# Kernel tuning notes

Measured on AMD Instinct MI355X. Metric: run time of the kernel, lower is better.

## Reference

```python
import jax, jax.numpy as jnp
import numpy as np

B, IMG, PATCH = 32, 128, 8
D, H, L, MLP, NC = 512, 8, 8, 2048, 3
P = (IMG // PATCH) ** 2  # 256 patches
N = P + 1                # +cls token
HD = D // H


def layer_norm(x, g, b, eps=1e-5):
    mu = jnp.mean(x, -1, keepdims=True)
    var = jnp.mean((x - mu) ** 2, -1, keepdims=True)
    return (x - mu) * jax.lax.rsqrt(var + eps) * g + b


def spt(x, w, b, g, beta):
    s = 1
    shifts = [x,
              jnp.roll(x, (s, s), (2, 3)),
              jnp.roll(x, (-s, s), (2, 3)),
              jnp.roll(x, (s, -s), (2, 3)),
              jnp.roll(x, (-s, -s), (2, 3))]
    xs = jnp.concatenate(shifts, axis=1)  # (B,5,H,W)
    y = jax.lax.conv_general_dilated(
        xs, w, (PATCH, PATCH), 'VALID',
        dimension_numbers=('NCHW', 'OIHW', 'NCHW')) + b[None, :, None, None]
    tok = y.reshape(y.shape[0], D, -1).transpose(0, 2, 1)  # (B,P,D)
    return layer_norm(tok, g, beta)


def block(tok, p):
    ln1g, ln1b, qkvw, qkvb, projw, projb, temp, ln2g, ln2b, w1, b1, w2, b2 = p
    x = layer_norm(tok, ln1g, ln1b)
    qkv = (x @ qkvw + qkvb).reshape(x.shape[0], N, 3, H, HD)
    q = jnp.transpose(qkv[:, :, 0], (0, 2, 1, 3))  # (B,H,N,HD)
    k = jnp.transpose(qkv[:, :, 1], (0, 2, 1, 3))
    v = jnp.transpose(qkv[:, :, 2], (0, 2, 1, 3))
    attn = jnp.einsum('bhnd,bhmd->bhnm', q, k) * temp[None, :, None, None]
    attn = jnp.where(jnp.eye(N, dtype=bool)[None, None], -jnp.inf, attn)
    attn = jax.nn.softmax(attn, -1)
    o = jnp.einsum('bhnm,bhmd->bhnd', attn, v)
    o = jnp.transpose(o, (0, 2, 1, 3)).reshape(x.shape[0], N, D)
    tok = tok + o @ projw + projb
    y = layer_norm(tok, ln2g, ln2b)
    y = jax.nn.gelu(y @ w1 + b1, approximate=False) @ w2 + b2
    return tok + y


def setup_inputs() -> dict:
    key = jax.random.key(0)
    ks = jax.random.split(key, 16)
    sc = 0.02
    inp = dict(
        image=jax.random.uniform(ks[0], (B, 1, IMG, IMG), jnp.float32),
        ssw=jax.random.normal(ks[1], (D, 5, PATCH, PATCH), jnp.float32) * sc,
        ssb=jnp.zeros((D,), jnp.float32),
        ssg=jnp.ones((D,), jnp.float32),
        ssbeta=jnp.zeros((D,), jnp.float32),
        sow=jax.random.normal(ks[2], (D, 5, PATCH, PATCH), jnp.float32) * sc,
        sob=jnp.zeros((D,), jnp.float32),
        sog=jnp.ones((D,), jnp.float32),
        sobeta=jnp.zeros((D,), jnp.float32),
        fw=jax.random.normal(ks[3], (2 * D, D), jnp.float32) * sc,
        fb=jnp.zeros((D,), jnp.float32),
        cls_token=jax.random.normal(ks[4], (1, 1, D), jnp.float32) * sc,
        pos_embed=jax.random.normal(ks[5], (1, N, D), jnp.float32) * sc,
        ln1g=jnp.ones((L, D), jnp.float32),
        ln1b=jnp.zeros((L, D), jnp.float32),
        qkvw=jax.random.normal(ks[6], (L, D, 3 * D), jnp.float32) * sc,
        qkvb=jnp.zeros((L, 3 * D), jnp.float32),
        projw=jax.random.normal(ks[7], (L, D, D), jnp.float32) * sc,
        projb=jnp.zeros((L, D), jnp.float32),
        temp=jnp.ones((L, H), jnp.float32) / np.sqrt(HD),
        ln2g=jnp.ones((L, D), jnp.float32),
        ln2b=jnp.zeros((L, D), jnp.float32),
        w1=jax.random.normal(ks[8], (L, D, MLP), jnp.float32) * sc,
        b1=jnp.zeros((L, MLP), jnp.float32),
        w2=jax.random.normal(ks[9], (L, MLP, D), jnp.float32) * sc,
        b2=jnp.zeros((L, D), jnp.float32),
        ng=jnp.ones((D,), jnp.float32),
        nb=jnp.zeros((D,), jnp.float32),
        hw=jax.random.normal(ks[10], (D, NC), jnp.float32) * sc,
        hb=jnp.zeros((NC,), jnp.float32),
    )
    return inp


def reference(image, ssw, ssb, ssg, ssbeta, sow, sob, sog, sobeta, fw, fb,
              cls_token, pos_embed, ln1g, ln1b, qkvw, qkvb, projw, projb,
              temp, ln2g, ln2b, w1, b1, w2, b2, ng, nb, hw, hb):
    # InverseLensLayer is undefined in the source repo snippet: identity
    source = image
    src_tok = spt(source, ssw, ssb, ssg, ssbeta)   # (B,P,D)
    orig_tok = spt(image, sow, sob, sog, sobeta)   # (B,P,D)
    comb = jnp.concatenate([src_tok, orig_tok], -1)
    gate = jax.nn.sigmoid(comb @ fw + fb)
    fused = gate * src_tok + (1.0 - gate) * orig_tok
    cls = jnp.broadcast_to(cls_token, (image.shape[0], 1, D))
    tokens = jnp.concatenate([cls, fused], axis=1) + pos_embed  # (B,N,D)

    def body(tok, p):
        return block(tok, p), None

    params = (ln1g, ln1b, qkvw, qkvb, projw, projb, temp,
              ln2g, ln2b, w1, b1, w2, b2)
    tokens, _ = jax.lax.scan(body, tokens, params)
    cls_out = layer_norm(tokens[:, 0], ng, nb)
    logits = cls_out @ hw + hb
    return logits
```

## Files before the change

### kernel.cpp

```cpp
#include <hip/hip_runtime.h>
#include <math.h>

constexpr int B_ = 32, D_ = 512, H_ = 8, L_ = 8, MLP_ = 2048, NC_ = 3;
constexpr int P_ = 256;
constexpr int N_ = 257;
constexpr int HD_ = 64;
constexpr int BP_ = B_ * P_;
constexpr int BN_ = B_ * N_;
constexpr int MP_ = 8320;
constexpr int KP_ = 320;
constexpr int NV_ = 288;

enum { EPI_BIAS = 0, EPI_RES = 1, EPI_GELU = 2 };

using bf16x8 = __attribute__((ext_vector_type(8))) short;
using f32x4  = __attribute__((ext_vector_type(4))) float;

__device__ __forceinline__ float b2f(unsigned short u) {
    return __uint_as_float(((unsigned)u) << 16);
}
__device__ __forceinline__ unsigned short f2b(float f) {
    unsigned u = __float_as_uint(f);
    unsigned r = (u + 0x7FFFu + ((u >> 16) & 1u)) >> 16;
    return (unsigned short)r;
}

__device__ __forceinline__ void gld_lds16(const void* g, void* l) {
    __builtin_amdgcn_global_load_lds(
        (const __attribute__((address_space(1))) void*)g,
        (__attribute__((address_space(3))) void*)l, 16, 0, 0);
}

__global__ void im2col_k(const float* __restrict__ img,
                         unsigned short* __restrict__ X) {
    int idx = blockIdx.x * 256 + threadIdx.x;
    if (idx >= BP_ * KP_) return;
    int r = idx / KP_, j = idx % KP_;
    int b = r >> 8, p = r & 255;
    int py = p >> 4, px = p & 15;
    int c = j >> 6, kk = j & 63;
    int ky = kk >> 3, kx = kk & 7;
    const int dy[5] = {0, 1, -1, 1, -1};
    const int dx[5] = {0, 1, 1, -1, -1};
    int yy = (py * 8 + ky - dy[c] + 128) & 127;
    int xx = (px * 8 + kx - dx[c] + 128) & 127;
    X[idx] = f2b(img[b * 16384 + yy * 128 + xx]);
}

__global__ __launch_bounds__(256) void castT_k(const float* __restrict__ in,
                                               unsigned short* __restrict__ out,
                                               int K, int N) {
    __shared__ float t[32][33];
    size_t loff = (size_t)blockIdx.z * K * N;
    int k0 = blockIdx.x * 32, n0 = blockIdx.y * 32;
    int tx = threadIdx.x & 31, ty = threadIdx.x >> 5;
    for (int i = ty; i < 32; i += 8)
        t[i][tx] = in[loff + (size_t)(k0 + i) * N + n0 + tx];
    __syncthreads();
    for (int i = ty; i < 32; i += 8)
        out[loff + (size_t)(n0 + i) * K + k0 + tx] = f2b(t[tx][i]);
}

__global__ void cast_k(const float* __restrict__ in,
                       unsigned short* __restrict__ out, int n) {
    int idx = blockIdx.x * 256 + threadIdx.x;
    if (idx < n) out[idx] = f2b(in[idx]);
}

__global__ __launch_bounds__(256) void gemm_bf16_k(
    const unsigned short* __restrict__ A, const unsigned short* __restrict__ Bt,
    const float* __restrict__ bias, const float* __restrict__ res,
    float* __restrict__ outF, unsigned short* __restrict__ outB,
    int Nn, int K, int epi) {
    constexpr int BK = 32;
    __shared__ unsigned short As[128 * BK];
    __shared__ unsigned short Bs[128 * BK];
    int tid = threadIdx.x, lane = tid & 63;
    int wave = tid >> 6;
    int wrow = (wave >> 1) * 64, wcol = (wave & 1) * 64;
    size_t bm = (size_t)blockIdx.y * 128, bn = (size_t)blockIdx.x * 128;
    const unsigned short* Ab = A + bm * K;
    const unsigned short* Bb = Bt + bn * K;

    f32x4 acc[4][4] = {};
    int quad = lane >> 4, col = lane & 15;
    int q8 = quad * 8;

    for (int k0 = 0; k0 < K; k0 += BK) {
#pragma unroll
        for (int it = 0; it < 2; ++it) {
            int c = it * 256 + tid;
            int row = c >> 2, cb = (c & 3) * 8;
            gld_lds16(Ab + (size_t)row * K + k0 + cb, (char*)As + c * 16);
            gld_lds16(Bb + (size_t)row * K + k0 + cb, (char*)Bs + c * 16);
        }
        __syncthreads();
        bf16x8 af[4], bfr[4];
#pragma unroll
        for (int i = 0; i < 4; ++i) {
            af[i]  = *(const bf16x8*)&As[(wrow + i * 16 + col) * BK + q8];
            bfr[i] = *(const bf16x8*)&Bs[(wcol + i * 16 + col) * BK + q8];
        }
#pragma unroll
        for (int mi = 0; mi < 4; ++mi)
#pragma unroll
            for (int ni = 0; ni < 4; ++ni)
                acc[mi][ni] = __builtin_amdgcn_mfma_f32_16x16x32_bf16(
                    af[mi], bfr[ni], acc[mi][ni], 0, 0, 0);
        __syncthreads();
    }

#pragma unroll
    for (int mi = 0; mi < 4; ++mi) {
#pragma unroll
        for (int ni = 0; ni < 4; ++ni) {
            size_t gm0 = bm + wrow + mi * 16 + quad * 4;
            size_t gn = bn + wcol + ni * 16 + col;
            float bs = bias ? bias[gn] : 0.f;
#pragma unroll
            for (int r = 0; r < 4; ++r) {
                size_t o = (gm0 + r) * Nn + gn;
                float v = acc[mi][ni][r] + bs;
                if (epi == EPI_GELU)
                    v = 0.5f * v * (1.f + erff(v * 0.70710678118654752f));
                else if (epi == EPI_RES)
                    v += res[o];
                if (outF) outF[o] = v;
                if (outB) outB[o] = f2b(v);
            }
        }
    }
}

__global__ __launch_bounds__(256) void ln_k(
    const float* __restrict__ in, float* __restrict__ outF,
    unsigned short* __restrict__ outB, const float* __restrict__ g,
    const float* __restrict__ be, long instride, long ofs, long obs) {
    __shared__ float red[256];
    int row = blockIdx.x;
    const float* x = in + (size_t)row * instride;
    int t = threadIdx.x;
    float v0 = x[t], v1 = x[t + 256];
    red[t] = v0 + v1;
    __syncthreads();
    for (int s = 128; s > 0; s >>= 1) {
        if (t < s) red[t] += red[t + s];
        __syncthreads();
    }
    float mu = red[0] * (1.f / 512.f);
    __syncthreads();
    float d0 = v0 - mu, d1 = v1 - mu;
    red[t] = d0 * d0 + d1 * d1;
    __syncthreads();
    for (int s = 128; s > 0; s >>= 1) {
        if (t < s) red[t] += red[t + s];
        __syncthreads();
    }
    float rs = rsqrtf(red[0] * (1.f / 512.f) + 1e-5f);
    float y0 = d0 * rs * g[t] + be[t];
    float y1 = d1 * rs * g[t + 256] + be[t + 256];
    if (outF) {
        float* y = outF + (size_t)row * ofs;
        y[t] = y0; y[t + 256] = y1;
    }
    if (outB) {
        unsigned short* y = outB + (size_t)row * obs;
        y[t] = f2b(y0); y[t + 256] = f2b(y1);
    }
}

__global__ void assemble_k(const float* __restrict__ gatelin,
                           const float* __restrict__ src,
                           const float* __restrict__ orig,
                           const float* __restrict__ cls,
                           const float* __restrict__ pos,
                           float* __restrict__ tokens) {
    int idx = blockIdx.x * 256 + threadIdx.x;
    if (idx >= B_ * N_ * D_) return;
    int d = idx & 511;
    int bn = idx >> 9;
    int b = bn / N_, n = bn % N_;
    float v;
    if (n == 0) {
        v = cls[d];
    } else {
        int r = b * 256 + (n - 1);
        float gl = gatelin[r * 512 + d];
        float g = 1.f / (1.f + expf(-gl));
        v = g * src[r * 512 + d] + (1.f - g) * orig[r * 512 + d];
    }
    tokens[idx] = v + pos[n * 512 + d];
}

__global__ __launch_bounds__(256) void vT_k(const unsigned short* __restrict__ qkv,
                                            unsigned short* __restrict__ Vt_g) {
    __shared__ unsigned short t[64][72];
    int bh = blockIdx.x, nt = blockIdx.y;
    int b = bh >> 3, h = bh & 7;
    int n0 = nt * 64;
    const unsigned short* vb = qkv + (size_t)(b * N_) * 1536 + 1024 + h * 64;
    int tid = threadIdx.x;
    for (int idx = tid; idx < 64 * 8; idx += 256) {
        int n = idx >> 3, c = idx & 7;
        int gn = n0 + n;
        uint4 u = {0, 0, 0, 0};
        if (gn < N_) u = *(const uint4*)(vb + (size_t)gn * 1536 + c * 8);
        *(uint4*)&t[n][c * 8] = u;
    }
    __syncthreads();
    for (int idx = tid; idx < 64 * 8; idx += 256) {
        int d = idx >> 3, j = idx & 7;
        if (n0 + j * 8 >= NV_) continue;
        unsigned short tmp[8];
#pragma unroll
        for (int e = 0; e < 8; ++e) tmp[e] = t[j * 8 + e][d];
        *(uint4*)&Vt_g[((size_t)bh * 64 + d) * NV_ + n0 + j * 8] =
            *(uint4*)tmp;
    }
}

__global__ __launch_bounds__(256) void attn_fused_k(
    const unsigned short* __restrict__ qkv,
    const unsigned short* __restrict__ Vt_g, const float* __restrict__ temp,
    unsigned short* __restrict__ obuf) {
    __shared__ __align__(16) unsigned short Ps[4][16][40];
    int bh = blockIdx.x;
    int b = bh >> 3, h = bh & 7;
    int tid = threadIdx.x, lane = tid & 63, wave = tid >> 6;
    int quad = lane >> 4, cid = lane & 15;
    int qt = blockIdx.y * 4 + wave;
    if (qt > 16) return;
    const unsigned short* qb = qkv + (size_t)(b * N_) * 1536 + h * 64;
    const unsigned short* kb = qb + 512;
    const unsigned short* vt = Vt_g + (size_t)bh * 64 * NV_;
    float tmp = temp[h];

    int qrow = qt * 16 + cid;
    if (qrow > 256) qrow = 256;
    bf16x8 aq0 = *(const bf16x8*)(qb + (size_t)qrow * 1536 + quad * 8);
    bf16x8 aq1 = *(const bf16x8*)(qb + (size_t)qrow * 1536 + 32 + quad * 8);

    f32x4 s[18];
#pragma unroll
    for (int t = 0; t < 17; ++t) {
        int krow = t * 16 + cid;
        if (t == 16 && krow > 256) krow = 256;
        const unsigned short* kp = kb + (size_t)krow * 1536 + quad * 8;
        bf16x8 bk0 = *(const bf16x8*)kp;
        bf16x8 bk1 = *(const bf16x8*)(kp + 32);
        f32x4 a = {0.f, 0.f, 0.f, 0.f};
        a = __builtin_amdgcn_mfma_f32_16x16x32_bf16(aq0, bk0, a, 0, 0, 0);
        a = __builtin_amdgcn_mfma_f32_16x16x32_bf16(aq1, bk1, a, 0, 0, 0);
        s[t] = a;
    }

    float mx[4] = {-1e30f, -1e30f, -1e30f, -1e30f};
#pragma unroll
    for (int t = 0; t < 17; ++t) {
        int col = t * 16 + cid;
#pragma unroll
        for (int r = 0; r < 4; ++r) {
            int row = qt * 16 + quad * 4 + r;
            float v = s[t][r] * tmp;
            if (col == row || col >= 257) v = -1e30f;
            s[t][r] = v;
            mx[r] = fmaxf(mx[r], v);
        }
    }
    s[17] = f32x4{-1e30f, -1e30f, -1e30f, -1e30f};
#pragma unroll
    for (int m = 1; m < 16; m <<= 1)
#pragma unroll
        for (int r = 0; r < 4; ++r) mx[r] = fmaxf(mx[r], __shfl_xor(mx[r], m));
    float sum[4] = {0.f, 0.f, 0.f, 0.f};
#pragma unroll
    for (int t = 0; t < 18; ++t)
#pragma unroll
        for (int r = 0; r < 4; ++r) {
            float e = __expf(s[t][r] - mx[r]);
            float ef = b2f(f2b(e));
            s[t][r] = ef;
            sum[r] += ef;
        }
#pragma unroll
    for (int m = 1; m < 16; m <<= 1)
#pragma unroll
        for (int r = 0; r < 4; ++r) sum[r] += __shfl_xor(sum[r], m);
    float inv[4];
#pragma unroll
    for (int r = 0; r < 4; ++r) inv[r] = 1.f / sum[r];

    f32x4 o[4] = {};
#pragma unroll
    for (int kt = 0; kt < 9; ++kt) {
#pragma unroll
        for (int hh = 0; hh < 2; ++hh) {
            int t = kt * 2 + hh;
#pragma unroll
            for (int r = 0; r < 4; ++r)
                Ps[wave][quad * 4 + r][hh * 16 + cid] = f2b(s[t][r]);
        }
        bf16x8 ap = *(const bf16x8*)&Ps[wave][cid][quad * 8];
#pragma unroll
        for (int dt = 0; dt < 4; ++dt) {
            bf16x8 bv = *(const bf16x8*)(vt + (size_t)(dt * 16 + cid) * NV_ +
                                         kt * 32 + quad * 8);
            o[dt] =
                __builtin_amdgcn_mfma_f32_16x16x32_bf16(ap, bv, o[dt], 0, 0, 0);
        }
    }
#pragma unroll
    for (int dt = 0; dt < 4; ++dt)
#pragma unroll
        for (int r = 0; r < 4; ++r) {
            int row = qt * 16 + quad * 4 + r;
            if (row < N_)
                obuf[(size_t)(b * N_ + row) * 512 + h * 64 + dt * 16 + cid] =
                    f2b(o[dt][r] * inv[r]);
        }
}

__global__ void head_k(const float* __restrict__ cls_out,
                       const float* __restrict__ hw,
                       const float* __restrict__ hb, float* __restrict__ out) {
    int t = threadIdx.x;
    if (t >= B_ * NC_) return;
    int b = t / NC_, c = t % NC_;
    float acc = hb[c];
    for (int d = 0; d < D_; ++d) acc += cls_out[b * D_ + d] * hw[d * NC_ + c];
    out[t] = acc;
}

extern "C" void kernel_launch(void* const* d_in, const int* in_sizes, int n_in,
                              void* d_out, int out_size, void* d_ws,
                              size_t ws_size, hipStream_t stream) {
    const float* image     = (const float*)d_in[0];
    const float* ssw       = (const float*)d_in[1];
    const float* ssb       = (const float*)d_in[2];
    const float* ssg       = (const float*)d_in[3];
    const float* ssbeta    = (const float*)d_in[4];
    const float* sow       = (const float*)d_in[5];
    const float* sob       = (const float*)d_in[6];
    const float* sog       = (const float*)d_in[7];
    const float* sobeta    = (const float*)d_in[8];
    const float* fw        = (const float*)d_in[9];
    const float* fb        = (const float*)d_in[10];
    const float* cls_token = (const float*)d_in[11];
    const float* pos_embed = (const float*)d_in[12];
    const float* ln1g      = (const float*)d_in[13];
    const float* ln1b      = (const float*)d_in[14];
    const float* qkvw      = (const float*)d_in[15];
    const float* qkvb      = (const float*)d_in[16];
    const float* projw     = (const float*)d_in[17];
    const float* projb     = (const float*)d_in[18];
    const float* temp      = (const float*)d_in[19];
    const float* ln2g      = (const float*)d_in[20];
    const float* ln2b      = (const float*)d_in[21];
    const float* w1        = (const float*)d_in[22];
    const float* b1        = (const float*)d_in[23];
    const float* w2        = (const float*)d_in[24];
    const float* b2        = (const float*)d_in[25];
    const float* ng        = (const float*)d_in[26];
    const float* nb        = (const float*)d_in[27];
    const float* hw        = (const float*)d_in[28];
    const float* hb        = (const float*)d_in[29];
    float* out = (float*)d_out;

    char* w = (char*)d_ws;
    size_t off = 0;
    float* tokens = (float*)w;                           off += (size_t)MP_ * 512 * 4;
    unsigned short* qkvw_t = (unsigned short*)(w + off); off += (size_t)8 * 1536 * 512 * 2;
    unsigned short* projw_t = (unsigned short*)(w + off); off += (size_t)8 * 512 * 512 * 2;
    unsigned short* w1_t = (unsigned short*)(w + off);   off += (size_t)8 * 2048 * 512 * 2;
    unsigned short* w2_t = (unsigned short*)(w + off);   off += (size_t)8 * 512 * 2048 * 2;
    unsigned short* fw_t = (unsigned short*)(w + off);   off += (size_t)512 * 1024 * 2;
    unsigned short* sswb = (unsigned short*)(w + off);   off += (size_t)512 * 320 * 2;
    unsigned short* sowb = (unsigned short*)(w + off);   off += (size_t)512 * 320 * 2;
    char* S = w + off;

    unsigned short* Xb   = (unsigned short*)S;
    float* srct          = (float*)(S + 5242880);
    float* origt         = (float*)(S + 5242880 + 16777216);
    unsigned short* comb = (unsigned short*)(S + 5242880 + 2 * 16777216);
    float* gatelin       = (float*)(S + 5242880 + 3 * 16777216);

    unsigned short* xbuf = (unsigned short*)S;
    unsigned short* qkvB = (unsigned short*)(S + 8519680);
    unsigned short* obuf = (unsigned short*)(S + 8519680 + 25559040);
    unsigned short* hbuf = (unsigned short*)(S + 8519680 + 25559040 + 8519680);
    unsigned short* vt_g = (unsigned short*)(S + 8519680 + 25559040 + 8519680 +
                                             34078720);
    float* cls_out = (float*)(S + 8519680 + 25559040 + 8519680 + 34078720 +
                              9437184);

    castT_k<<<dim3(16, 48, 8), 256, 0, stream>>>(qkvw, qkvw_t, 512, 1536);
    castT_k<<<dim3(16, 16, 8), 256, 0, stream>>>(projw, projw_t, 512, 512);
    castT_k<<<dim3(16, 64, 8), 256, 0, stream>>>(w1, w1_t, 512, 2048);
    castT_k<<<dim3(64, 16, 8), 256, 0, stream>>>(w2, w2_t, 2048, 512);
    castT_k<<<dim3(32, 16, 1), 256, 0, stream>>>(fw, fw_t, 1024, 512);
    cast_k<<<640, 256, 0, stream>>>(ssw, sswb, 512 * 320);
    cast_k<<<640, 256, 0, stream>>>(sow, sowb, 512 * 320);

    im2col_k<<<(BP_ * KP_ + 255) / 256, 256, 0, stream>>>(image, Xb);
    dim3 gspt(4, 64);
    gemm_bf16_k<<<gspt, 256, 0, stream>>>(Xb, sswb, ssb, nullptr, srct, nullptr,
                                          512, KP_, EPI_BIAS);
    ln_k<<<BP_, 256, 0, stream>>>(srct, srct, comb, ssg, ssbeta, 512, 512, 1024);
    gemm_bf16_k<<<gspt, 256, 0, stream>>>(Xb, sowb, sob, nullptr, origt, nullptr,
                                          512, KP_, EPI_BIAS);
    ln_k<<<BP_, 256, 0, stream>>>(origt, origt, comb + 512, sog, sobeta, 512,
                                  512, 1024);
    gemm_bf16_k<<<gspt, 256, 0, stream>>>(comb, fw_t, fb, nullptr, gatelin,
                                          nullptr, 512, 1024, EPI_BIAS);
    assemble_k<<<(B_ * N_ * D_ + 255) / 256, 256, 0, stream>>>(
        gatelin, srct, origt, cls_token, pos_embed, tokens);

    dim3 gqkv(12, 65), gproj(4, 65), gfc1(16, 65);
    for (int l = 0; l < L_; ++l) {
        const float* l1g = ln1g + l * D_;
        const float* l1b = ln1b + l * D_;
        const unsigned short* qw = qkvw_t + (size_t)l * 1536 * 512;
        const float* qb  = qkvb + (size_t)l * 3 * D_;
        const unsigned short* pw = projw_t + (size_t)l * 512 * 512;
        const float* pb  = projb + (size_t)l * D_;
        const float* tp  = temp + l * H_;
        const float* l2g = ln2g + l * D_;
        const float* l2b = ln2b + l * D_;
        const unsigned short* w1l = w1_t + (size_t)l * 2048 * 512;
        const float* b1l = b1 + (size_t)l * MLP_;
        const unsigned short* w2l = w2_t + (size_t)l * 512 * 2048;
        const float* b2l = b2 + (size_t)l * D_;

        ln_k<<<BN_, 256, 0, stream>>>(tokens, nullptr, xbuf, l1g, l1b, 512, 0,
                                      512);
        gemm_bf16_k<<<gqkv, 256, 0, stream>>>(xbuf, qw, qb, nullptr, nullptr,
                                              qkvB, 1536, 512, EPI_BIAS);
        vT_k<<<dim3(256, 5), 256, 0, stream>>>(qkvB, vt_g);
        attn_fused_k<<<dim3(256, 5), 256, 0, stream>>>(qkvB, vt_g, tp, obuf);
        gemm_bf16_k<<<gproj, 256, 0, stream>>>(obuf, pw, pb, tokens, tokens,
                                               nullptr, 512, 512, EPI_RES);
        ln_k<<<BN_, 256, 0, stream>>>(tokens, nullptr, xbuf, l2g, l2b, 512, 0,
                                      512);
        gemm_bf16_k<<<gfc1, 256, 0, stream>>>(xbuf, w1l, b1l, nullptr, nullptr,
                                              hbuf, 2048, 512, EPI_GELU);
        gemm_bf16_k<<<gproj, 256, 0, stream>>>(hbuf, w2l, b2l, tokens, tokens,
                                               nullptr, 512, 2048, EPI_RES);
    }

    ln_k<<<B_, 256, 0, stream>>>(tokens, cls_out, nullptr, ng, nb,
                                 (long)N_ * 512, 512, 0);
    head_k<<<1, 128, 0, stream>>>(cls_out, hw, hb, out);
}
```

Before: 2.524 ms.

## Rework bf16 GEMM with XOR-swizzled LDS, BK=64 and wider tiles

Replaces the bf16 MFMA GEMM with a templated version. The K-step is doubled to 64, and LDS holds 16-byte chunks in an XOR-swizzled layout, so MFMA fragment reads avoid bank conflicts. The QKV and FC1 GEMMs move to a 128x256 tile with 512 threads (8 waves), which halves the block count and raises B-tile reuse. In exchange, fewer blocks are launched per GEMM and LDS use per block grows, which may lower occupancy or cause wave-quantization effects.

```diff
diff --git a/kernel.cpp b/kernel.cpp
--- a/kernel.cpp
+++ b/kernel.cpp
@@ -67,46 +67,70 @@
     if (idx < n) out[idx] = f2b(in[idx]);
 }
 
-__global__ __launch_bounds__(256) void gemm_bf16_k(
+template <int TNT, int NTHR>
+__global__ __launch_bounds__(NTHR) void gemm2_k(
     const unsigned short* __restrict__ A, const unsigned short* __restrict__ Bt,
     const float* __restrict__ bias, const float* __restrict__ res,
     float* __restrict__ outF, unsigned short* __restrict__ outB,
     int Nn, int K, int epi) {
-    constexpr int BK = 32;
+    constexpr int BK = 64;
+    constexpr int NW = NTHR / 64;
+    constexpr int NWC = NW / 2;
+    constexpr int ACH = 128 * 8;
+    constexpr int BCH = TNT * 8;
     __shared__ unsigned short As[128 * BK];
-    __shared__ unsigned short Bs[128 * BK];
-    int tid = threadIdx.x, lane = tid & 63;
-    int wave = tid >> 6;
-    int wrow = (wave >> 1) * 64, wcol = (wave & 1) * 64;
-    size_t bm = (size_t)blockIdx.y * 128, bn = (size_t)blockIdx.x * 128;
+    __shared__ unsigned short Bs[TNT * BK];
+    int tid = threadIdx.x, lane = tid & 63, wave = tid >> 6;
+    int quad = lane >> 4, cid = lane & 15;
+    int wrow = (wave / NWC) * 64, wcol = (wave % NWC) * 64;
+    size_t bm = (size_t)blockIdx.y * 128, bn = (size_t)blockIdx.x * TNT;
     const unsigned short* Ab = A + bm * K;
     const unsigned short* Bb = Bt + bn * K;
 
     f32x4 acc[4][4] = {};
-    int quad = lane >> 4, col = lane & 15;
-    int q8 = quad * 8;
 
     for (int k0 = 0; k0 < K; k0 += BK) {
 #pragma unroll
-        for (int it = 0; it < 2; ++it) {
-            int c = it * 256 + tid;
-            int row = c >> 2, cb = (c & 3) * 8;
-            gld_lds16(Ab + (size_t)row * K + k0 + cb, (char*)As + c * 16);
-            gld_lds16(Bb + (size_t)row * K + k0 + cb, (char*)Bs + c * 16);
+        for (int c0 = 0; c0 < ACH; c0 += NTHR) {
+            int c = c0 + tid;
+            int row = c >> 3, j = c & 7;
+            int k8 = j ^ (row & 7);
+            int cw = c0 + (tid & ~63);
+            gld_lds16(Ab + (size_t)row * K + k0 + k8 * 8,
+                      (char*)As + cw * 16);
+        }
+#pragma unroll
+        for (int c0 = 0; c0 < BCH; c0 += NTHR) {
+            int c = c0 + tid;
+            int row = c >> 3, j = c & 7;
+            int k8 = j ^ (row & 7);
+            int cw = c0 + (tid & ~63);
+            gld_lds16(Bb + (size_t)row * K + k0 + k8 * 8,
+                      (char*)Bs + cw * 16);
         }
         __syncthreads();
-        bf16x8 af[4], bfr[4];
-#pragma unroll
-        for (int i = 0; i < 4; ++i) {
-            af[i]  = *(const bf16x8*)&As[(wrow + i * 16 + col) * BK + q8];
-            bfr[i] = *(const bf16x8*)&Bs[(wcol + i * 16 + col) * BK + q8];
-        }
-#pragma unroll
-        for (int mi = 0; mi < 4; ++mi)
-#pragma unroll
-            for (int ni = 0; ni < 4; ++ni)
-                acc[mi][ni] = __builtin_amdgcn_mfma_f32_16x16x32_bf16(
-                    af[mi], bfr[ni], acc[mi][ni], 0, 0, 0);
+#pragma unroll
+        for (int ks = 0; ks < 2; ++ks) {
+            bf16x8 af[4], bfr[4];
+#pragma unroll
+            for (int i = 0; i < 4; ++i) {
+                int r = wrow + i * 16 + cid;
+                int j = (ks * 4 + quad) ^ (r & 7);
+                af[i] = *(const bf16x8*)&As[(r * 8 + j) * 8];
+            }
+#pragma unroll
+            for (int i = 0; i < 4; ++i) {
+                int r = wcol + i * 16 + cid;
+                int j = (ks * 4 + quad) ^ (r & 7);
+                bfr[i] = *(const bf16x8*)&Bs[(r * 8 + j) * 8];
+            }
+#pragma unroll
+            for (int mi = 0; mi < 4; ++mi)
+#pragma unroll
+                for (int ni = 0; ni < 4; ++ni)
+                    acc[mi][ni] = __builtin_amdgcn_mfma_f32_16x16x32_bf16(
+                        af[mi], bfr[ni], acc[mi][ni], 0, 0, 0);
+        }
         __syncthreads();
     }
 
@@ -115,7 +139,7 @@
 #pragma unroll
         for (int ni = 0; ni < 4; ++ni) {
             size_t gm0 = bm + wrow + mi * 16 + quad * 4;
-            size_t gn = bn + wcol + ni * 16 + col;
+            size_t gn = bn + wcol + ni * 16 + cid;
             float bs = bias ? bias[gn] : 0.f;
 #pragma unroll
             for (int r = 0; r < 4; ++r) {
@@ -403,19 +427,20 @@
 
     im2col_k<<<(BP_ * KP_ + 255) / 256, 256, 0, stream>>>(image, Xb);
     dim3 gspt(4, 64);
-    gemm_bf16_k<<<gspt, 256, 0, stream>>>(Xb, sswb, ssb, nullptr, srct, nullptr,
-                                          512, KP_, EPI_BIAS);
+    gemm2_k<128, 256><<<gspt, 256, 0, stream>>>(Xb, sswb, ssb, nullptr, srct,
+                                                nullptr, 512, KP_, EPI_BIAS);
     ln_k<<<BP_, 256, 0, stream>>>(srct, srct, comb, ssg, ssbeta, 512, 512, 1024);
-    gemm_bf16_k<<<gspt, 256, 0, stream>>>(Xb, sowb, sob, nullptr, origt, nullptr,
-                                          512, KP_, EPI_BIAS);
+    gemm2_k<128, 256><<<gspt, 256, 0, stream>>>(Xb, sowb, sob, nullptr, origt,
+                                                nullptr, 512, KP_, EPI_BIAS);
     ln_k<<<BP_, 256, 0, stream>>>(origt, origt, comb + 512, sog, sobeta, 512,
                                   512, 1024);
-    gemm_bf16_k<<<gspt, 256, 0, stream>>>(comb, fw_t, fb, nullptr, gatelin,
-                                          nullptr, 512, 1024, EPI_BIAS);
+    gemm2_k<128, 256><<<gspt, 256, 0, stream>>>(comb, fw_t, fb, nullptr,
+                                                gatelin, nullptr, 512, 1024,
+                                                EPI_BIAS);
     assemble_k<<<(B_ * N_ * D_ + 255) / 256, 256, 0, stream>>>(
         gatelin, srct, origt, cls_token, pos_embed, tokens);
 
-    dim3 gqkv(12, 65), gproj(4, 65), gfc1(16, 65);
+    dim3 gqkv(6, 65), gproj(4, 65), gfc1(8, 65), gfc2(4, 65);
     for (int l = 0; l < L_; ++l) {
         const float* l1g = ln1g + l * D_;
         const float* l1b = ln1b + l * D_;
@@ -433,18 +458,22 @@
 
         ln_k<<<BN_, 256, 0, stream>>>(tokens, nullptr, xbuf, l1g, l1b, 512, 0,
                                       512);
-        gemm_bf16_k<<<gqkv, 256, 0, stream>>>(xbuf, qw, qb, nullptr, nullptr,
-                                              qkvB, 1536, 512, EPI_BIAS);
+        gemm2_k<256, 512><<<gqkv, 512, 0, stream>>>(xbuf, qw, qb, nullptr,
+                                                    nullptr, qkvB, 1536, 512,
+                                                    EPI_BIAS);
         vT_k<<<dim3(256, 5), 256, 0, stream>>>(qkvB, vt_g);
         attn_fused_k<<<dim3(256, 5), 256, 0, stream>>>(qkvB, vt_g, tp, obuf);
-        gemm_bf16_k<<<gproj, 256, 0, stream>>>(obuf, pw, pb, tokens, tokens,
-                                               nullptr, 512, 512, EPI_RES);
+        gemm2_k<128, 256><<<gproj, 256, 0, stream>>>(obuf, pw, pb, tokens,
+                                                     tokens, nullptr, 512, 512,
+                                                     EPI_RES);
         ln_k<<<BN_, 256, 0, stream>>>(tokens, nullptr, xbuf, l2g, l2b, 512, 0,
                                       512);
-        gemm_bf16_k<<<gfc1, 256, 0, stream>>>(xbuf, w1l, b1l, nullptr, nullptr,
-                                              hbuf, 2048, 512, EPI_GELU);
-        gemm_bf16_k<<<gproj, 256, 0, stream>>>(hbuf, w2l, b2l, tokens, tokens,
-                                               nullptr, 512, 2048, EPI_RES);
+        gemm2_k<256, 512><<<gfc1, 512, 0, stream>>>(xbuf, w1l, b1l, nullptr,
+                                                    nullptr, hbuf, 2048, 512,
+                                                    EPI_GELU);
+        gemm2_k<128, 256><<<gfc2, 256, 0, stream>>>(hbuf, w2l, b2l, tokens,
+                                                    tokens, nullptr, 512, 2048,
+                                                    EPI_RES);
     }
 
     ln_k<<<B_, 256, 0, stream>>>(tokens, cls_out, nullptr, ng, nb,
```

New measurement: 2.559 ms. No clear change (+1.4%).

## Replace LDS-staged GEMM with register double-buffered direct loads and grouped block swizzle

Applied to the files above, without the earlier changes.

The GEMM no longer stages tiles through shared memory with barriers. Each wave now loads its MFMA fragments straight from global memory into registers, double-buffered across K steps, and K becomes a template parameter so the loop fully unrolls. Blocks are remapped in groups of 8 rows for better L2 reuse, and the grid is padded to 72 with early exit. Dropping LDS removes the barriers, but it also loses sharing between waves: every wave reloads its A and B rows, which multiplies global and L2 traffic.

```diff
diff --git a/kernel.cpp b/kernel.cpp
--- a/kernel.cpp
+++ b/kernel.cpp
@@ -23,12 +23,6 @@
     unsigned u = __float_as_uint(f);
     unsigned r = (u + 0x7FFFu + ((u >> 16) & 1u)) >> 16;
     return (unsigned short)r;
-}
-
-__device__ __forceinline__ void gld_lds16(const void* g, void* l) {
-    __builtin_amdgcn_global_load_lds(
-        (const __attribute__((address_space(1))) void*)g,
-        (__attribute__((address_space(3))) void*)l, 16, 0, 0);
 }
 
 __global__ void im2col_k(const float* __restrict__ img,
@@ -67,47 +61,52 @@
     if (idx < n) out[idx] = f2b(in[idx]);
 }
 
-__global__ __launch_bounds__(256) void gemm_bf16_k(
+template <int K>
+__global__ __launch_bounds__(256) void gemmr_k(
     const unsigned short* __restrict__ A, const unsigned short* __restrict__ Bt,
     const float* __restrict__ bias, const float* __restrict__ res,
     float* __restrict__ outF, unsigned short* __restrict__ outB,
-    int Nn, int K, int epi) {
-    constexpr int BK = 32;
-    __shared__ unsigned short As[128 * BK];
-    __shared__ unsigned short Bs[128 * BK];
-    int tid = threadIdx.x, lane = tid & 63;
-    int wave = tid >> 6;
+    int Nn, int epi, int GYt) {
+    int GX = gridDim.x;
+    int flat = blockIdx.y * GX + blockIdx.x;
+    int grp = flat / (8 * GX), s = flat % (8 * GX);
+    int by = (s & 7) + 8 * grp;
+    int bx = s >> 3;
+    if (by >= GYt) return;
+
+    int tid = threadIdx.x, lane = tid & 63, wave = tid >> 6;
+    int quad = lane >> 4, cid = lane & 15;
     int wrow = (wave >> 1) * 64, wcol = (wave & 1) * 64;
-    size_t bm = (size_t)blockIdx.y * 128, bn = (size_t)blockIdx.x * 128;
-    const unsigned short* Ab = A + bm * K;
-    const unsigned short* Bb = Bt + bn * K;
+    size_t bm = (size_t)by * 128, bn = (size_t)bx * 128;
+    const unsigned short* Ap = A + (bm + wrow + cid) * K + quad * 8;
+    const unsigned short* Bp = Bt + (bn + wcol + cid) * K + quad * 8;
 
     f32x4 acc[4][4] = {};
-    int quad = lane >> 4, col = lane & 15;
-    int q8 = quad * 8;
-
-    for (int k0 = 0; k0 < K; k0 += BK) {
-#pragma unroll
-        for (int it = 0; it < 2; ++it) {
-            int c = it * 256 + tid;
-            int row = c >> 2, cb = (c & 3) * 8;
-            gld_lds16(Ab + (size_t)row * K + k0 + cb, (char*)As + c * 16);
-            gld_lds16(Bb + (size_t)row * K + k0 + cb, (char*)Bs + c * 16);
-        }
-        __syncthreads();
-        bf16x8 af[4], bfr[4];
-#pragma unroll
-        for (int i = 0; i < 4; ++i) {
-            af[i]  = *(const bf16x8*)&As[(wrow + i * 16 + col) * BK + q8];
-            bfr[i] = *(const bf16x8*)&Bs[(wcol + i * 16 + col) * BK + q8];
+    constexpr int NK = K / 32;
+    bf16x8 af[2][4], bfr[2][4];
+#pragma unroll
+    for (int i = 0; i < 4; ++i) {
+        af[0][i]  = *(const bf16x8*)(Ap + (size_t)i * 16 * K);
+        bfr[0][i] = *(const bf16x8*)(Bp + (size_t)i * 16 * K);
+    }
+#pragma unroll
+    for (int k = 0; k < NK; ++k) {
+        int cur = k & 1, nxt = cur ^ 1;
+        if (k + 1 < NK) {
+#pragma unroll
+            for (int i = 0; i < 4; ++i) {
+                af[nxt][i] =
+                    *(const bf16x8*)(Ap + (size_t)i * 16 * K + (k + 1) * 32);
+                bfr[nxt][i] =
+                    *(const bf16x8*)(Bp + (size_t)i * 16 * K + (k + 1) * 32);
+            }
         }
 #pragma unroll
         for (int mi = 0; mi < 4; ++mi)
 #pragma unroll
             for (int ni = 0; ni < 4; ++ni)
                 acc[mi][ni] = __builtin_amdgcn_mfma_f32_16x16x32_bf16(
-                    af[mi], bfr[ni], acc[mi][ni], 0, 0, 0);
-        __syncthreads();
+                    af[cur][mi], bfr[cur][ni], acc[mi][ni], 0, 0, 0);
     }
 
 #pragma unroll
@@ -115,7 +114,7 @@
 #pragma unroll
         for (int ni = 0; ni < 4; ++ni) {
             size_t gm0 = bm + wrow + mi * 16 + quad * 4;
-            size_t gn = bn + wcol + ni * 16 + col;
+            size_t gn = bn + wcol + ni * 16 + cid;
             float bs = bias ? bias[gn] : 0.f;
 #pragma unroll
             for (int r = 0; r < 4; ++r) {
@@ -403,19 +402,19 @@
 
     im2col_k<<<(BP_ * KP_ + 255) / 256, 256, 0, stream>>>(image, Xb);
     dim3 gspt(4, 64);
-    gemm_bf16_k<<<gspt, 256, 0, stream>>>(Xb, sswb, ssb, nullptr, srct, nullptr,
-                                          512, KP_, EPI_BIAS);
+    gemmr_k<KP_><<<gspt, 256, 0, stream>>>(Xb, sswb, ssb, nullptr, srct,
+                                           nullptr, 512, EPI_BIAS, 64);
     ln_k<<<BP_, 256, 0, stream>>>(srct, srct, comb, ssg, ssbeta, 512, 512, 1024);
-    gemm_bf16_k<<<gspt, 256, 0, stream>>>(Xb, sowb, sob, nullptr, origt, nullptr,
-                                          512, KP_, EPI_BIAS);
+    gemmr_k<KP_><<<gspt, 256, 0, stream>>>(Xb, sowb, sob, nullptr, origt,
+                                           nullptr, 512, EPI_BIAS, 64);
     ln_k<<<BP_, 256, 0, stream>>>(origt, origt, comb + 512, sog, sobeta, 512,
                                   512, 1024);
-    gemm_bf16_k<<<gspt, 256, 0, stream>>>(comb, fw_t, fb, nullptr, gatelin,
-                                          nullptr, 512, 1024, EPI_BIAS);
+    gemmr_k<1024><<<gspt, 256, 0, stream>>>(comb, fw_t, fb, nullptr, gatelin,
+                                            nullptr, 512, EPI_BIAS, 64);
     assemble_k<<<(B_ * N_ * D_ + 255) / 256, 256, 0, stream>>>(
         gatelin, srct, origt, cls_token, pos_embed, tokens);
 
-    dim3 gqkv(12, 65), gproj(4, 65), gfc1(16, 65);
+    dim3 gqkv(12, 72), gproj(4, 72), gfc1(16, 72), gfc2(4, 72);
     for (int l = 0; l < L_; ++l) {
         const float* l1g = ln1g + l * D_;
         const float* l1b = ln1b + l * D_;
@@ -433,18 +432,18 @@
 
         ln_k<<<BN_, 256, 0, stream>>>(tokens, nullptr, xbuf, l1g, l1b, 512, 0,
                                       512);
-        gemm_bf16_k<<<gqkv, 256, 0, stream>>>(xbuf, qw, qb, nullptr, nullptr,
-                                              qkvB, 1536, 512, EPI_BIAS);
+        gemmr_k<512><<<gqkv, 256, 0, stream>>>(xbuf, qw, qb, nullptr, nullptr,
+                                               qkvB, 1536, EPI_BIAS, 65);
         vT_k<<<dim3(256, 5), 256, 0, stream>>>(qkvB, vt_g);
         attn_fused_k<<<dim3(256, 5), 256, 0, stream>>>(qkvB, vt_g, tp, obuf);
-        gemm_bf16_k<<<gproj, 256, 0, stream>>>(obuf, pw, pb, tokens, tokens,
-                                               nullptr, 512, 512, EPI_RES);
+        gemmr_k<512><<<gproj, 256, 0, stream>>>(obuf, pw, pb, tokens, tokens,
+                                                nullptr, 512, EPI_RES, 65);
         ln_k<<<BN_, 256, 0, stream>>>(tokens, nullptr, xbuf, l2g, l2b, 512, 0,
                                       512);
-        gemm_bf16_k<<<gfc1, 256, 0, stream>>>(xbuf, w1l, b1l, nullptr, nullptr,
-                                              hbuf, 2048, 512, EPI_GELU);
-        gemm_bf16_k<<<gproj, 256, 0, stream>>>(hbuf, w2l, b2l, tokens, tokens,
-                                               nullptr, 512, 2048, EPI_RES);
+        gemmr_k<512><<<gfc1, 256, 0, stream>>>(xbuf, w1l, b1l, nullptr, nullptr,
+                                               hbuf, 2048, EPI_GELU, 65);
+        gemmr_k<2048><<<gfc2, 256, 0, stream>>>(hbuf, w2l, b2l, tokens, tokens,
+                                                nullptr, 512, EPI_RES, 65);
     }
 
     ln_k<<<B_, 256, 0, stream>>>(tokens, cls_out, nullptr, ng, nb,
```

After: 3.826 ms. 1.52x slower.
